# Optimization experiments

Hardware: AMD Instinct MI355X
Metric: run time of the kernel (lower is better)

The kernel has to match this reference:

```python
import jax, jax.numpy as jnp
from jax import lax
import numpy as np

EPS = 1e-06


def conv1x1(x, W, b):
    # x: [B,C,H,W], W: [O,C], b: [O]
    return jnp.einsum('bchw,oc->bohw', x, W) + b[None, :, None, None]


def conv3x3(x, W, b):
    # W: [O,I,3,3], 'SAME' padding
    y = lax.conv_general_dilated(x, W, (1, 1), 'SAME',
                                 dimension_numbers=('NCHW', 'OIHW', 'NCHW'))
    return y + b[None, :, None, None]


def setup_inputs() -> dict:
    key = jax.random.key(0)
    ks = jax.random.split(key, 13)
    B, C, H, W = 8, 64, 256, 256
    kc, vc = 64, 64
    s = 0.05
    return {
        'x':  jax.random.normal(ks[0], (B, C, H, W), jnp.float32),
        'Wq': jax.random.normal(ks[1], (kc, C), jnp.float32) * s,
        'bq': jax.random.normal(ks[2], (kc,), jnp.float32) * s,
        'Wk': jax.random.normal(ks[3], (kc, C), jnp.float32) * s,
        'bk': jax.random.normal(ks[4], (kc,), jnp.float32) * s,
        'Wv': jax.random.normal(ks[5], (vc, C), jnp.float32) * s,
        'bv': jax.random.normal(ks[6], (vc,), jnp.float32) * s,
        'Wr': jax.random.normal(ks[7], (C, vc), jnp.float32) * s,
        'br': jax.random.normal(ks[8], (C,), jnp.float32) * s,
        'W1': jax.random.normal(ks[9], (C, C, 3, 3), jnp.float32) * s,
        'b1': jax.random.normal(ks[10], (C,), jnp.float32) * s,
        'W2': jax.random.normal(ks[11], (C, C, 3, 3), jnp.float32) * s,
        'b2': jax.random.normal(ks[12], (C,), jnp.float32) * s,
    }


def reference(x, Wq, bq, Wk, bk, Wv, bv, Wr, br, W1, b1, W2, b2):
    B, C, H, W = x.shape
    N = H * W
    kc = Wq.shape[0]
    vc = Wv.shape[0]

    Q = conv1x1(x, Wq, bq).reshape(B, kc, N)
    K = conv1x1(x, Wk, bk).reshape(B, kc, N)
    V = conv1x1(x, Wv, bv).reshape(B, vc, N)

    # L2-normalize over the channel axis (dim=-2 in torch)
    Qn = Q / jnp.linalg.norm(Q, axis=1, keepdims=True)   # [B,kc,N]
    Kn = K / jnp.linalg.norm(K, axis=1, keepdims=True)   # [B,kc,N]
    Qt = jnp.transpose(Qn, (0, 2, 1))                     # [B,N,kc]

    # denominator: 1 / (N + Q . (sum_n K + eps))
    k_sum = Kn.sum(axis=-1) + EPS                         # [B,kc]
    denom = 1.0 / (N + jnp.einsum('bnc,bc->bn', Qt, k_sum))  # [B,N]

    value_sum = V.sum(axis=-1, keepdims=True)             # [B,vc,1]

    # linear-attention aggregation: KV^T then Q.(KV)
    agg_kv = jnp.einsum('bmn,bcn->bmc', Kn, V)            # [B,kc,vc]
    # the per-batch/per-head torch loop sums head slices of the full kc
    # contraction -> equivalent to a single einsum over kc
    agg_qkv = jnp.einsum('bmc,bnm->bcn', agg_kv, Qt)      # [B,vc,N]

    numerator = value_sum + agg_qkv                       # [B,vc,N]
    weight_value = (numerator * denom[:, None, :]).reshape(B, vc, H, W)

    attn = conv1x1(weight_value, Wr, br)                  # [B,C,H,W]
    out = conv3x3(conv3x3(attn, W1, b1), W2, b2) * x + x
    return out
```

## Files before the change

### kernel.cpp

```cpp
#include <hip/hip_runtime.h>

typedef __attribute__((ext_vector_type(8))) short short8;
typedef __attribute__((ext_vector_type(4))) float f32x4;
typedef __attribute__((ext_vector_type(4))) int i32x4;

#define NPIX 65536
#define KPITCH 264
#define RED_KSUM 0
#define RED_VSUM 512
#define RED_AGG 1024

__device__ __forceinline__ float b2f(unsigned short u) {
  union { unsigned int i; float f; } z; z.i = ((unsigned int)u) << 16; return z.f;
}
__device__ __forceinline__ unsigned short f2b(float f) {
  union { float f; unsigned int i; } z; z.f = f;
  unsigned int r = z.i + 0x7fffu + ((z.i >> 16) & 1u);
  return (unsigned short)(r >> 16);
}
__device__ __forceinline__ unsigned int packbf(float a, float b) {
  return (unsigned int)f2b(a) | ((unsigned int)f2b(b) << 16);
}
__device__ __forceinline__ int cvtpk(float a, float b) {
  int r;
  asm("v_cvt_pk_bf16_f32 %0, %1, %2" : "=v"(r) : "v"(a), "v"(b));
  return r;
}

__global__ __launch_bounds__(256) void prep_kernel(
    const float* __restrict__ W1, const float* __restrict__ W2,
    unsigned short* __restrict__ wA, float* __restrict__ red)
{
  const int i = blockIdx.x * 256 + threadIdx.x;
  if (i < 73728) {
    const float* W = (i < 36864) ? W1 : W2;
    const int e = (i < 36864) ? i : (i - 36864);
    const int j    = e & 7;
    const int lane = (e >> 3) & 63;
    const int mt   = (e >> 9) & 3;
    const int kb   = (e >> 11) & 1;
    const int tap  = e >> 12;
    const int o = mt * 16 + (lane & 15);
    const int c = kb * 32 + ((lane >> 4) << 3) + j;
    wA[i] = f2b(W[o * 576 + c * 9 + tap]);
  } else if (i < 73728 + 33792) {
    red[i - 73728] = 0.0f;
  }
}

#define PROJ(WM, BM)                                                           \
    {                                                                          \
      _Pragma("unroll")                                                        \
      for (int mt = 0; mt < 4; ++mt) {                                         \
        const f32x4 bb = *(const f32x4*)((BM) + mt * 16 + g * 4);              \
        _Pragma("unroll")                                                      \
        for (int nt = 0; nt < 4; ++nt) acc[mt][nt] = bb;                       \
      }                                                                        \
      _Pragma("unroll")                                                        \
      for (int kb = 0; kb < 2; ++kb) {                                         \
        short8 af[4];                                                          \
        _Pragma("unroll")                                                      \
        for (int mt = 0; mt < 4; ++mt) {                                       \
          const float* wp = (WM) + mt * 1024 + wrow + kb * 32;                 \
          const f32x4 w0 = *(const f32x4*)wp;                                  \
          const f32x4 w1 = *(const f32x4*)(wp + 4);                            \
          union { i32x4 i; short8 s; } uw;                                     \
          uw.i.x = cvtpk(w0.x, w0.y); uw.i.y = cvtpk(w0.z, w0.w);              \
          uw.i.z = cvtpk(w1.x, w1.y); uw.i.w = cvtpk(w1.z, w1.w);              \
          af[mt] = uw.s;                                                       \
        }                                                                      \
        _Pragma("unroll")                                                      \
        for (int mt = 0; mt < 4; ++mt)                                         \
          _Pragma("unroll")                                                    \
          for (int nt = 0; nt < 4; ++nt)                                       \
            acc[mt][nt] = __builtin_amdgcn_mfma_f32_16x16x32_bf16(             \
                af[mt], bf[nt][kb], acc[mt][nt], 0, 0, 0);                     \
      }                                                                        \
    }

__global__ __launch_bounds__(256, 2) void qkv_kernel(
    const float* __restrict__ x,
    const float* __restrict__ Wq, const float* __restrict__ bq,
    const float* __restrict__ Wk, const float* __restrict__ bk,
    const float* __restrict__ Wv, const float* __restrict__ bv,
    unsigned short* __restrict__ Qn, float* __restrict__ red)
{
  __shared__ __align__(16) unsigned short sh[2 * 64 * KPITCH];
  unsigned short* ks = sh;
  unsigned short* vs = sh + 64 * KPITCH;
  unsigned int* shu = (unsigned int*)sh;
  const int b = blockIdx.y;
  const int t = threadIdx.x;
  const int w = t >> 6;
  const int l = t & 63;
  const int g = l >> 4;
  const int l15 = l & 15;
  const int wrow = l15 * 64 + g * 8;
  const size_t xb = (size_t)b * 64 * NPIX;

  const f32x4 zero = {0.f, 0.f, 0.f, 0.f};
  f32x4 agg[4]  = {zero, zero, zero, zero};
  f32x4 kacc[4] = {zero, zero, zero, zero};
  f32x4 vacc[4] = {zero, zero, zero, zero};

  for (int it = 0; it < 4; ++it) {
    const int pxw = (blockIdx.x << 10) + (it << 8) + (w << 6);

    short8 bf[4][2];
#pragma unroll
    for (int nt = 0; nt < 4; ++nt) {
      const float* xp = x + xb + (size_t)(g * 8) * NPIX + pxw + nt * 16 + l15;
#pragma unroll
      for (int kb = 0; kb < 2; ++kb) {
        float f[8];
#pragma unroll
        for (int j = 0; j < 8; ++j)
          f[j] = xp[(size_t)(kb * 32 + j) * NPIX];
        union { i32x4 i; short8 s; } u;
        u.i.x = cvtpk(f[0], f[1]); u.i.y = cvtpk(f[2], f[3]);
        u.i.z = cvtpk(f[4], f[5]); u.i.w = cvtpk(f[6], f[7]);
        bf[nt][kb] = u.s;
      }
    }

    f32x4 acc[4][4];

    PROJ(Wq, bq);
    {
      float rq[4];
#pragma unroll
      for (int nt = 0; nt < 4; ++nt) {
        float ss = 0.f;
#pragma unroll
        for (int mt = 0; mt < 4; ++mt)
#pragma unroll
          for (int r = 0; r < 4; ++r)
            ss = fmaf(acc[mt][nt][r], acc[mt][nt][r], ss);
        ss += __shfl_xor(ss, 16);
        ss += __shfl_xor(ss, 32);
        rq[nt] = rsqrtf(ss);
      }
      unsigned int* sw = shu + w * 2304;
#pragma unroll
      for (int mt = 0; mt < 4; ++mt)
#pragma unroll
        for (int nt = 0; nt < 4; ++nt) {
          const int px = nt * 16 + l15;
          unsigned int* dst = sw + px * 36 + mt * 8 + g * 2;
          dst[0] = (unsigned)cvtpk(acc[mt][nt][0] * rq[nt], acc[mt][nt][1] * rq[nt]);
          dst[1] = (unsigned)cvtpk(acc[mt][nt][2] * rq[nt], acc[mt][nt][3] * rq[nt]);
        }
      const uint4* rr4 = (const uint4*)(shu + w * 2304);
#pragma unroll
      for (int k8 = 0; k8 < 8; ++k8) {
        const int p = (k8 << 3) + (l >> 3);
        const int ch8 = l & 7;
        *(uint4*)(Qn + ((size_t)b * NPIX + pxw + p) * 64 + ch8 * 8) =
            rr4[p * 9 + ch8];
      }
      __syncthreads();
    }

    PROJ(Wk, bk);
    {
      float rk[4];
#pragma unroll
      for (int nt = 0; nt < 4; ++nt) {
        float ss = 0.f;
#pragma unroll
        for (int mt = 0; mt < 4; ++mt)
#pragma unroll
          for (int r = 0; r < 4; ++r)
            ss = fmaf(acc[mt][nt][r], acc[mt][nt][r], ss);
        ss += __shfl_xor(ss, 16);
        ss += __shfl_xor(ss, 32);
        rk[nt] = rsqrtf(ss);
      }
#pragma unroll
      for (int mt = 0; mt < 4; ++mt)
#pragma unroll
        for (int nt = 0; nt < 4; ++nt)
#pragma unroll
          for (int r = 0; r < 4; ++r) {
            const float kn = acc[mt][nt][r] * rk[nt];
            kacc[mt][r] += kn;
            ks[(mt * 16 + g * 4 + r) * KPITCH + (w << 6) + nt * 16 + l15] =
                (unsigned short)cvtpk(kn, 0.f);
          }
    }

    PROJ(Wv, bv);
    {
#pragma unroll
      for (int mt = 0; mt < 4; ++mt)
#pragma unroll
        for (int nt = 0; nt < 4; ++nt)
#pragma unroll
          for (int r = 0; r < 4; ++r) {
            const float vv = acc[mt][nt][r];
            vacc[mt][r] += vv;
            vs[(mt * 16 + g * 4 + r) * KPITCH + (w << 6) + nt * 16 + l15] =
                (unsigned short)cvtpk(vv, 0.f);
          }
    }
    __syncthreads();

#pragma unroll
    for (int s = 0; s < 8; ++s) {
      const short8 ak =
          *(const short8*)(ks + (w * 16 + l15) * KPITCH + s * 32 + g * 8);
#pragma unroll
      for (int nt = 0; nt < 4; ++nt) {
        const short8 bv8 =
            *(const short8*)(vs + (nt * 16 + l15) * KPITCH + s * 32 + g * 8);
        agg[nt] = __builtin_amdgcn_mfma_f32_16x16x32_bf16(ak, bv8, agg[nt], 0, 0, 0);
      }
    }
    __syncthreads();
  }

#pragma unroll
  for (int mt = 0; mt < 4; ++mt)
#pragma unroll
    for (int r = 0; r < 4; ++r) {
      float kv = kacc[mt][r], vv = vacc[mt][r];
#pragma unroll
      for (int d = 1; d < 16; d <<= 1) {
        kv += __shfl_xor(kv, d);
        vv += __shfl_xor(vv, d);
      }
      if (l15 == 0) {
        atomicAdd(red + RED_KSUM + b * 64 + mt * 16 + g * 4 + r, kv);
        atomicAdd(red + RED_VSUM + b * 64 + mt * 16 + g * 4 + r, vv);
      }
    }
  float* ab = red + RED_AGG + b * 4096;
#pragma unroll
  for (int nt = 0; nt < 4; ++nt)
#pragma unroll
    for (int r = 0; r < 4; ++r)
      atomicAdd(ab + (w * 16 + g * 4 + r) * 64 + nt * 16 + l15, agg[nt][r]);
}

__global__ __launch_bounds__(256) void prep2_kernel(
    const float* __restrict__ Wr, const float* __restrict__ red,
    unsigned short* __restrict__ Cb, float* __restrict__ u,
    float* __restrict__ ks2)
{
  const int b = blockIdx.y;
  const int t = threadIdx.x;
  const int o = t & 63;
  const int kq = t >> 6;
  const float* wr = Wr + o * 64;
  const float* agg = red + RED_AGG + b * 4096;
#pragma unroll
  for (int i = 0; i < 4; ++i) {
    const int k = blockIdx.x * 16 + kq * 4 + i;
    const float* ar = agg + k * 64;
    float s = 0.f;
#pragma unroll
    for (int v = 0; v < 64; ++v) s = fmaf(wr[v], ar[v], s);
    const int mt = o >> 4, kb = k >> 5;
    const int lane = (o & 15) | (((k >> 3) & 3) << 4);
    const int j = k & 7;
    const unsigned short c1 = f2b(s);
    const float r1 = s - b2f(c1);
    Cb[b * 4096 + ((kb * 4 + mt) * 64 + lane) * 8 + j] = c1;
    Cb[32768 + b * 4096 + ((kb * 4 + mt) * 64 + lane) * 8 + j] = f2b(r1);
  }
  if (blockIdx.x == 0 && t < 64) {
    const float* vsr = red + RED_VSUM + b * 64;
    float s = 0.f;
#pragma unroll
    for (int v = 0; v < 64; ++v) s = fmaf(Wr[t * 64 + v], vsr[v], s);
    u[b * 64 + t] = s;
    ks2[b * 64 + t] = red[RED_KSUM + b * 64 + t] + 1e-6f;
  }
}

__global__ __launch_bounds__(256, 2) void attn_kernel(
    const unsigned short* __restrict__ Qn,
    const unsigned short* __restrict__ Cb,
    const float* __restrict__ u,
    const float* __restrict__ ks2,
    const float* __restrict__ br,
    unsigned short* __restrict__ attn)
{
  __shared__ __align__(16) unsigned short att[256 * 72];
  const int b = blockIdx.y;
  const int t = threadIdx.x;
  const int w = t >> 6, l = t & 63, g = l >> 4, l15 = l & 15;

  short8 af[2][2][4];
#pragma unroll
  for (int lvl = 0; lvl < 2; ++lvl)
#pragma unroll
    for (int kb = 0; kb < 2; ++kb)
#pragma unroll
      for (int mt = 0; mt < 4; ++mt)
        af[lvl][kb][mt] = *(const short8*)(
            Cb + lvl * 32768 + b * 4096 + ((kb * 4 + mt) * 64 + l) * 8);
  f32x4 uu[4], brf[4];
#pragma unroll
  for (int mt = 0; mt < 4; ++mt) {
    uu[mt]  = *(const f32x4*)(u + b * 64 + mt * 16 + g * 4);
    brf[mt] = *(const f32x4*)(br + mt * 16 + g * 4);
  }
  float ksl[16];
#pragma unroll
  for (int kb = 0; kb < 2; ++kb)
#pragma unroll
    for (int j = 0; j < 8; ++j)
      ksl[kb * 8 + j] = ks2[b * 64 + kb * 32 + g * 8 + j];

  for (int it = 0; it < 4; ++it) {
    const int pxw = (blockIdx.x << 10) + (it << 8) + (w << 6);
    short8 qf[4][2];
    float denom[4];
#pragma unroll
    for (int nt = 0; nt < 4; ++nt) {
      const unsigned short* qp =
          Qn + ((size_t)b * NPIX + pxw + nt * 16 + l15) * 64 + g * 8;
      qf[nt][0] = *(const short8*)qp;
      qf[nt][1] = *(const short8*)(qp + 32);
      float ss = 0.f;
#pragma unroll
      for (int kb = 0; kb < 2; ++kb)
#pragma unroll
        for (int j = 0; j < 8; ++j)
          ss = fmaf(b2f((unsigned short)qf[nt][kb][j]), ksl[kb * 8 + j], ss);
      ss += __shfl_xor(ss, 16);
      ss += __shfl_xor(ss, 32);
      denom[nt] = 1.0f / (65536.0f + ss);
    }
    f32x4 acc[4][4];
#pragma unroll
    for (int mt = 0; mt < 4; ++mt)
#pragma unroll
      for (int nt = 0; nt < 4; ++nt) acc[mt][nt] = uu[mt];
#pragma unroll
    for (int kb = 0; kb < 2; ++kb)
#pragma unroll
      for (int mt = 0; mt < 4; ++mt)
#pragma unroll
        for (int nt = 0; nt < 4; ++nt) {
          acc[mt][nt] = __builtin_amdgcn_mfma_f32_16x16x32_bf16(
              af[0][kb][mt], qf[nt][kb], acc[mt][nt], 0, 0, 0);
          acc[mt][nt] = __builtin_amdgcn_mfma_f32_16x16x32_bf16(
              af[1][kb][mt], qf[nt][kb], acc[mt][nt], 0, 0, 0);
        }
    unsigned int* sw = (unsigned int*)att + w * 2304;
#pragma unroll
    for (int mt = 0; mt < 4; ++mt)
#pragma unroll
      for (int nt = 0; nt < 4; ++nt) {
        const int px = nt * 16 + l15;
        unsigned int* dst = sw + px * 36 + mt * 8 + g * 2;
        dst[0] = (unsigned)cvtpk(fmaf(acc[mt][nt][0], denom[nt], brf[mt][0]),
                                 fmaf(acc[mt][nt][1], denom[nt], brf[mt][1]));
        dst[1] = (unsigned)cvtpk(fmaf(acc[mt][nt][2], denom[nt], brf[mt][2]),
                                 fmaf(acc[mt][nt][3], denom[nt], brf[mt][3]));
      }
    const uint4* rr4 = (const uint4*)att + w * 576;
#pragma unroll
    for (int k8 = 0; k8 < 8; ++k8) {
      const int p = (k8 << 3) + (l >> 3);
      const int ch8 = l & 7;
      *(uint4*)(attn + ((size_t)b * NPIX + pxw + p) * 64 + ch8 * 8) =
          rr4[p * 9 + ch8];
    }
  }
}

template <int EPI>
__global__ __launch_bounds__(256, 3) void conv3_kernel(
    const unsigned short* __restrict__ in,
    const unsigned short* __restrict__ wA,
    const float* __restrict__ bias,
    const float* __restrict__ xin,
    unsigned short* __restrict__ outh,
    float* __restrict__ outf)
{
  __shared__ __align__(16) unsigned short tile[10 * 34 * 72];
  const int bz = blockIdx.z;
  const int ty0 = blockIdx.y << 3;
  const int tx0 = blockIdx.x << 5;
  const int tid = threadIdx.x;
  const size_t nb = (size_t)bz * NPIX;

  for (int s = tid; s < 2720; s += 256) {
    const int g = s & 7;
    const int pix = s >> 3;
    const int xx = pix % 34;
    const int row = pix / 34;
    const int gx = tx0 + xx - 1;
    const int gy = ty0 + row - 1;
    uint4 v = {0u, 0u, 0u, 0u};
    if ((unsigned)gx < 256u && (unsigned)gy < 256u)
      v = *(const uint4*)(in + ((nb + (gy << 8) + gx) << 6) + (g << 3));
    *(uint4*)(tile + pix * 72 + (g << 3)) = v;
  }
  __syncthreads();

  const int w = tid >> 6, lane = tid & 63, q = lane >> 4, l = lane & 15;
  f32x4 acc[4][4];
  {
#pragma unroll
    for (int mt = 0; mt < 4; ++mt) {
      const f32x4 bb = *(const f32x4*)(bias + mt * 16 + q * 4);
#pragma unroll
      for (int nt = 0; nt < 4; ++nt) acc[mt][nt] = bb;
    }
  }
  const short8* tp = (const short8*)tile;
  for (int tap = 0; tap < 9; ++tap) {
    const int dy = tap / 3, dx = tap - dy * 3;
#pragma unroll
    for (int kb = 0; kb < 2; ++kb) {
      const unsigned short* wp = wA + (tap * 2 + kb) * 2048 + lane * 8;
      short8 af[4];
#pragma unroll
      for (int mt = 0; mt < 4; ++mt) af[mt] = *(const short8*)(wp + mt * 512);
      short8 bf[4];
#pragma unroll
      for (int nt = 0; nt < 4; ++nt) {
        const int yl = (w << 1) + (nt >> 1) + dy;
        const int xl = ((nt & 1) << 4) + l + dx;
        bf[nt] = tp[(yl * 34 + xl) * 9 + (kb << 2) + q];
      }
#pragma unroll
      for (int mt = 0; mt < 4; ++mt)
#pragma unroll
        for (int nt = 0; nt < 4; ++nt)
          acc[mt][nt] = __builtin_amdgcn_mfma_f32_16x16x32_bf16(
              af[mt], bf[nt], acc[mt][nt], 0, 0, 0);
    }
  }

  if (EPI == 0) {
    __syncthreads();
    unsigned int* wreg = (unsigned int*)tile + w * 2304;
#pragma unroll
    for (int mt = 0; mt < 4; ++mt)
#pragma unroll
      for (int nt = 0; nt < 4; ++nt) {
        const int p = ((nt >> 1) << 5) + ((nt & 1) << 4) + l;
        unsigned int* dst = wreg + p * 36 + (mt << 3) + (q << 1);
        dst[0] = packbf(acc[mt][nt][0], acc[mt][nt][1]);
        dst[1] = packbf(acc[mt][nt][2], acc[mt][nt][3]);
      }
    __syncthreads();
    const uint4* rreg = (const uint4*)tile + w * 576;
#pragma unroll
    for (int k = 0; k < 8; ++k) {
      const int p = (k << 3) + (lane >> 3);
      const int ch = lane & 7;
      const int gx = tx0 + (p & 31);
      const int gy = ty0 + (w << 1) + (p >> 5);
      *(uint4*)(outh + ((nb + (gy << 8) + gx) << 6) + (ch << 3)) =
          rreg[p * 9 + ch];
    }
  } else {
#pragma unroll
    for (int mt = 0; mt < 4; ++mt)
#pragma unroll
      for (int nt = 0; nt < 4; ++nt) {
        const int gx = tx0 + ((nt & 1) << 4) + l;
        const int gy = ty0 + (w << 1) + (nt >> 1);
#pragma unroll
        for (int r = 0; r < 4; ++r) {
          const int o = (mt << 4) + (q << 2) + r;
          const size_t idx = (((size_t)bz * 64 + o) << 16) + (gy << 8) + gx;
          const float xo = xin[idx];
          outf[idx] = fmaf(acc[mt][nt][r], xo, xo);
        }
      }
  }
}

extern "C" void kernel_launch(void* const* d_in, const int* in_sizes, int n_in,
                              void* d_out, int out_size, void* d_ws, size_t ws_size,
                              hipStream_t stream) {
  (void)in_sizes; (void)n_in; (void)out_size; (void)ws_size;
  const float* x  = (const float*)d_in[0];
  const float* Wq = (const float*)d_in[1];
  const float* bq = (const float*)d_in[2];
  const float* Wk = (const float*)d_in[3];
  const float* bk = (const float*)d_in[4];
  const float* Wv = (const float*)d_in[5];
  const float* bv = (const float*)d_in[6];
  const float* Wr = (const float*)d_in[7];
  const float* br = (const float*)d_in[8];
  const float* W1 = (const float*)d_in[9];
  const float* b1 = (const float*)d_in[10];
  const float* W2 = (const float*)d_in[11];
  const float* b2 = (const float*)d_in[12];

  unsigned short* wA1 = (unsigned short*)d_ws;
  unsigned short* wA2 = wA1 + 36864;
  float* red = (float*)((char*)d_ws + 147456);
  unsigned short* bufA = (unsigned short*)((char*)d_ws + 294912);
  unsigned short* Cb = (unsigned short*)((char*)d_ws + 294912);
  float* u_  = (float*)((char*)d_ws + 294912 + 131072);
  float* ks2 = (float*)((char*)d_ws + 294912 + 133120);
  unsigned short* bufB = (unsigned short*)d_out;
  unsigned short* bufQ = (unsigned short*)((char*)d_out + 67108864);

  prep_kernel<<<420, 256, 0, stream>>>(W1, W2, wA1, red);
  qkv_kernel<<<dim3(64, 8), 256, 0, stream>>>(x, Wq, bq, Wk, bk, Wv, bv, bufQ, red);
  prep2_kernel<<<dim3(4, 8), 256, 0, stream>>>(Wr, red, Cb, u_, ks2);
  attn_kernel<<<dim3(64, 8), 256, 0, stream>>>(bufQ, Cb, u_, ks2, br, bufB);
  conv3_kernel<0><<<dim3(8, 32, 8), 256, 0, stream>>>(
      bufB, wA1, b1, nullptr, bufA, nullptr);
  conv3_kernel<1><<<dim3(8, 32, 8), 256, 0, stream>>>(
      bufA, wA2, b2, x, nullptr, (float*)d_out);
}
```

Before: 599.1 us.

## Eliminate V projection by aggregating x-weighted K norms and folding Wv in prep2

The qkv kernel no longer computes the V projection or stores normalized K and V in shared memory. Instead it accumulates M = sum over pixels of (x scaled by 1/||K||) times x^T, plus per-channel sums, and prep2 reconstructs agg_kv, k_sum and value_sum algebraically through Wk, Wv, bk and bv. This removes a projection's worth of MFMA work and a large shared-memory staging buffer, which lets occupancy rise to 3 blocks per CU. In exchange it re-reads x from global memory, changes the bf16 rounding points, and makes prep2 a serial 8-block matrix chain.

```diff
diff --git a/kernel.cpp b/kernel.cpp
--- a/kernel.cpp
+++ b/kernel.cpp
@@ -5,10 +5,10 @@
 typedef __attribute__((ext_vector_type(4))) int i32x4;
 
 #define NPIX 65536
-#define KPITCH 264
-#define RED_KSUM 0
-#define RED_VSUM 512
+#define RED_M1 0
+#define RED_MX 512
 #define RED_AGG 1024
+#define RED_S1 33792
 
 __device__ __forceinline__ float b2f(unsigned short u) {
   union { unsigned int i; float f; } z; z.i = ((unsigned int)u) << 16; return z.f;
@@ -43,7 +43,7 @@
     const int o = mt * 16 + (lane & 15);
     const int c = kb * 32 + ((lane >> 4) << 3) + j;
     wA[i] = f2b(W[o * 576 + c * 9 + tap]);
-  } else if (i < 73728 + 33792) {
+  } else if (i < 73728 + 33800) {
     red[i - 73728] = 0.0f;
   }
 }
@@ -78,33 +78,27 @@
       }                                                                        \
     }
 
-__global__ __launch_bounds__(256, 2) void qkv_kernel(
+__global__ __launch_bounds__(256, 3) void qkv_kernel(
     const float* __restrict__ x,
     const float* __restrict__ Wq, const float* __restrict__ bq,
     const float* __restrict__ Wk, const float* __restrict__ bk,
-    const float* __restrict__ Wv, const float* __restrict__ bv,
     unsigned short* __restrict__ Qn, float* __restrict__ red)
 {
-  __shared__ __align__(16) unsigned short sh[2 * 64 * KPITCH];
-  unsigned short* ks = sh;
-  unsigned short* vs = sh + 64 * KPITCH;
-  unsigned int* shu = (unsigned int*)sh;
+  __shared__ __align__(16) unsigned short qsc[4 * 2304];
+  __shared__ __align__(16) float dkbuf[256];
   const int b = blockIdx.y;
   const int t = threadIdx.x;
-  const int w = t >> 6;
-  const int l = t & 63;
-  const int g = l >> 4;
-  const int l15 = l & 15;
+  const int w = t >> 6, l = t & 63, g = l >> 4, l15 = l & 15;
   const int wrow = l15 * 64 + g * 8;
   const size_t xb = (size_t)b * 64 * NPIX;
 
   const f32x4 zero = {0.f, 0.f, 0.f, 0.f};
-  f32x4 agg[4]  = {zero, zero, zero, zero};
-  f32x4 kacc[4] = {zero, zero, zero, zero};
-  f32x4 vacc[4] = {zero, zero, zero, zero};
+  f32x4 Mw[4] = {zero, zero, zero, zero};
+  float m1p = 0.f, mxp = 0.f, s1p = 0.f;
 
   for (int it = 0; it < 4; ++it) {
-    const int pxw = (blockIdx.x << 10) + (it << 8) + (w << 6);
+    const int pxblk = (blockIdx.x << 10) + (it << 8);
+    const int pxw = pxblk + (w << 6);
 
     short8 bf[4][2];
 #pragma unroll
@@ -140,25 +134,29 @@
         ss += __shfl_xor(ss, 32);
         rq[nt] = rsqrtf(ss);
       }
-      unsigned int* sw = shu + w * 2304;
-#pragma unroll
-      for (int mt = 0; mt < 4; ++mt)
-#pragma unroll
-        for (int nt = 0; nt < 4; ++nt) {
-          const int px = nt * 16 + l15;
-          unsigned int* dst = sw + px * 36 + mt * 8 + g * 2;
-          dst[0] = (unsigned)cvtpk(acc[mt][nt][0] * rq[nt], acc[mt][nt][1] * rq[nt]);
-          dst[1] = (unsigned)cvtpk(acc[mt][nt][2] * rq[nt], acc[mt][nt][3] * rq[nt]);
+      unsigned int* sw = (unsigned int*)qsc + w * 1152;
+#pragma unroll
+      for (int h = 0; h < 2; ++h) {
+#pragma unroll
+        for (int mt = 0; mt < 4; ++mt)
+#pragma unroll
+          for (int n2 = 0; n2 < 2; ++n2) {
+            const int nt = h * 2 + n2;
+            unsigned int* dst = sw + (n2 * 16 + l15) * 36 + mt * 8 + g * 2;
+            dst[0] = (unsigned)cvtpk(acc[mt][nt][0] * rq[nt],
+                                     acc[mt][nt][1] * rq[nt]);
+            dst[1] = (unsigned)cvtpk(acc[mt][nt][2] * rq[nt],
+                                     acc[mt][nt][3] * rq[nt]);
+          }
+        const uint4* rr4 = (const uint4*)qsc + w * 288;
+#pragma unroll
+        for (int k4 = 0; k4 < 4; ++k4) {
+          const int p = (k4 << 3) + (l >> 3);
+          const int ch8 = l & 7;
+          *(uint4*)(Qn + ((size_t)b * NPIX + pxw + h * 32 + p) * 64 + ch8 * 8) =
+              rr4[p * 9 + ch8];
         }
-      const uint4* rr4 = (const uint4*)(shu + w * 2304);
-#pragma unroll
-      for (int k8 = 0; k8 < 8; ++k8) {
-        const int p = (k8 << 3) + (l >> 3);
-        const int ch8 = l & 7;
-        *(uint4*)(Qn + ((size_t)b * NPIX + pxw + p) * 64 + ch8 * 8) =
-            rr4[p * 9 + ch8];
-      }
-      __syncthreads();
+      }
     }
 
     PROJ(Wk, bk);
@@ -176,105 +174,135 @@
         ss += __shfl_xor(ss, 32);
         rk[nt] = rsqrtf(ss);
       }
-#pragma unroll
-      for (int mt = 0; mt < 4; ++mt)
+      s1p += rk[0] + rk[1] + rk[2] + rk[3];
+      if (l < 16) {
 #pragma unroll
         for (int nt = 0; nt < 4; ++nt)
-#pragma unroll
-          for (int r = 0; r < 4; ++r) {
-            const float kn = acc[mt][nt][r] * rk[nt];
-            kacc[mt][r] += kn;
-            ks[(mt * 16 + g * 4 + r) * KPITCH + (w << 6) + nt * 16 + l15] =
-                (unsigned short)cvtpk(kn, 0.f);
-          }
-    }
-
-    PROJ(Wv, bv);
-    {
-#pragma unroll
-      for (int mt = 0; mt < 4; ++mt)
-#pragma unroll
-        for (int nt = 0; nt < 4; ++nt)
-#pragma unroll
-          for (int r = 0; r < 4; ++r) {
-            const float vv = acc[mt][nt][r];
-            vacc[mt][r] += vv;
-            vs[(mt * 16 + g * 4 + r) * KPITCH + (w << 6) + nt * 16 + l15] =
-                (unsigned short)cvtpk(vv, 0.f);
-          }
+          dkbuf[(w << 6) + nt * 16 + l15] = rk[nt];
+      }
     }
     __syncthreads();
 
 #pragma unroll
     for (int s = 0; s < 8; ++s) {
-      const short8 ak =
-          *(const short8*)(ks + (w * 16 + l15) * KPITCH + s * 32 + g * 8);
-#pragma unroll
-      for (int nt = 0; nt < 4; ++nt) {
-        const short8 bv8 =
-            *(const short8*)(vs + (nt * 16 + l15) * KPITCH + s * 32 + g * 8);
-        agg[nt] = __builtin_amdgcn_mfma_f32_16x16x32_bf16(ak, bv8, agg[nt], 0, 0, 0);
+      const int pk = pxblk + s * 32 + g * 8;
+      const float* xa = x + xb + (size_t)(w * 16 + l15) * NPIX + pk;
+      const f32x4 a0 = *(const f32x4*)xa;
+      const f32x4 a1 = *(const f32x4*)(xa + 4);
+      const f32x4 d0 = *(const f32x4*)(dkbuf + s * 32 + g * 8);
+      const f32x4 d1 = *(const f32x4*)(dkbuf + s * 32 + g * 8 + 4);
+      const float p0 = a0.x * d0.x, p1 = a0.y * d0.y;
+      const float p2 = a0.z * d0.z, p3 = a0.w * d0.w;
+      const float p4 = a1.x * d1.x, p5 = a1.y * d1.y;
+      const float p6 = a1.z * d1.z, p7 = a1.w * d1.w;
+      m1p += p0 + p1 + p2 + p3 + p4 + p5 + p6 + p7;
+      mxp += a0.x + a0.y + a0.z + a0.w + a1.x + a1.y + a1.z + a1.w;
+      union { i32x4 i; short8 s8; } ua;
+      ua.i.x = cvtpk(p0, p1); ua.i.y = cvtpk(p2, p3);
+      ua.i.z = cvtpk(p4, p5); ua.i.w = cvtpk(p6, p7);
+#pragma unroll
+      for (int nt = 0; nt < 4; ++nt) {
+        const float* xbp = x + xb + (size_t)(nt * 16 + l15) * NPIX + pk;
+        const f32x4 b0 = *(const f32x4*)xbp;
+        const f32x4 b1 = *(const f32x4*)(xbp + 4);
+        union { i32x4 i; short8 s8; } ub;
+        ub.i.x = cvtpk(b0.x, b0.y); ub.i.y = cvtpk(b0.z, b0.w);
+        ub.i.z = cvtpk(b1.x, b1.y); ub.i.w = cvtpk(b1.z, b1.w);
+        Mw[nt] = __builtin_amdgcn_mfma_f32_16x16x32_bf16(
+            ua.s8, ub.s8, Mw[nt], 0, 0, 0);
       }
     }
     __syncthreads();
   }
 
-#pragma unroll
-  for (int mt = 0; mt < 4; ++mt)
-#pragma unroll
-    for (int r = 0; r < 4; ++r) {
-      float kv = kacc[mt][r], vv = vacc[mt][r];
-#pragma unroll
-      for (int d = 1; d < 16; d <<= 1) {
-        kv += __shfl_xor(kv, d);
-        vv += __shfl_xor(vv, d);
-      }
-      if (l15 == 0) {
-        atomicAdd(red + RED_KSUM + b * 64 + mt * 16 + g * 4 + r, kv);
-        atomicAdd(red + RED_VSUM + b * 64 + mt * 16 + g * 4 + r, vv);
-      }
-    }
-  float* ab = red + RED_AGG + b * 4096;
+  m1p += __shfl_xor(m1p, 16); m1p += __shfl_xor(m1p, 32);
+  mxp += __shfl_xor(mxp, 16); mxp += __shfl_xor(mxp, 32);
+  if (l < 16) {
+    atomicAdd(red + RED_M1 + b * 64 + w * 16 + l15, m1p);
+    atomicAdd(red + RED_MX + b * 64 + w * 16 + l15, mxp);
+  }
+  s1p += __shfl_xor(s1p, 1); s1p += __shfl_xor(s1p, 2);
+  s1p += __shfl_xor(s1p, 4); s1p += __shfl_xor(s1p, 8);
+  if (l == 0) atomicAdd(red + RED_S1 + b, s1p);
+  float* Mb = red + RED_AGG + b * 4096;
 #pragma unroll
   for (int nt = 0; nt < 4; ++nt)
 #pragma unroll
     for (int r = 0; r < 4; ++r)
-      atomicAdd(ab + (w * 16 + g * 4 + r) * 64 + nt * 16 + l15, agg[nt][r]);
+      atomicAdd(Mb + (w * 16 + g * 4 + r) * 64 + nt * 16 + l15, Mw[nt][r]);
 }
 
 __global__ __launch_bounds__(256) void prep2_kernel(
+    const float* __restrict__ Wk, const float* __restrict__ bk,
+    const float* __restrict__ Wv, const float* __restrict__ bv,
     const float* __restrict__ Wr, const float* __restrict__ red,
     unsigned short* __restrict__ Cb, float* __restrict__ u,
     float* __restrict__ ks2)
 {
-  const int b = blockIdx.y;
+  __shared__ float T[4096];
+  __shared__ float P2[4096];
+  __shared__ float sm[320];
+  const int b = blockIdx.x;
   const int t = threadIdx.x;
-  const int o = t & 63;
-  const int kq = t >> 6;
-  const float* wr = Wr + o * 64;
-  const float* agg = red + RED_AGG + b * 4096;
-#pragma unroll
-  for (int i = 0; i < 4; ++i) {
-    const int k = blockIdx.x * 16 + kq * 4 + i;
-    const float* ar = agg + k * 64;
-    float s = 0.f;
-#pragma unroll
-    for (int v = 0; v < 64; ++v) s = fmaf(wr[v], ar[v], s);
-    const int mt = o >> 4, kb = k >> 5;
-    const int lane = (o & 15) | (((k >> 3) & 3) << 4);
-    const int j = k & 7;
-    const unsigned short c1 = f2b(s);
-    const float r1 = s - b2f(c1);
-    Cb[b * 4096 + ((kb * 4 + mt) * 64 + lane) * 8 + j] = c1;
-    Cb[32768 + b * 4096 + ((kb * 4 + mt) * 64 + lane) * 8 + j] = f2b(r1);
-  }
-  if (blockIdx.x == 0 && t < 64) {
-    const float* vsr = red + RED_VSUM + b * 64;
-    float s = 0.f;
-#pragma unroll
-    for (int v = 0; v < 64; ++v) s = fmaf(Wr[t * 64 + v], vsr[v], s);
-    u[b * 64 + t] = s;
-    ks2[b * 64 + t] = red[RED_KSUM + b * 64 + t] + 1e-6f;
+  const float* M  = red + RED_AGG + b * 4096;
+  const float* m1 = red + RED_M1 + b * 64;
+  const float* mx = red + RED_MX + b * 64;
+  const float s1 = red[RED_S1 + b];
+  if (t < 64) {
+    float a = 0.f, c = 0.f, d = 0.f;
+    for (int v = 0; v < 64; ++v) {
+      a = fmaf(Wk[t * 64 + v], m1[v], a);
+      c = fmaf(Wv[t * 64 + v], m1[v], c);
+      d = fmaf(Wv[t * 64 + v], mx[v], d);
+    }
+    sm[t] = a;
+    sm[64 + t] = c;
+    sm[128 + t] = d;
+  }
+  __syncthreads();
+  {
+    const int o = t & 63, n0 = (t >> 6) * 16;
+    for (int n = n0; n < n0 + 16; ++n) {
+      float s = 0.f;
+      for (int v = 0; v < 64; ++v) s = fmaf(Wv[o * 64 + v], M[v * 64 + n], s);
+      T[o * 64 + n] = s;
+    }
+  }
+  __syncthreads();
+  {
+    const int o = t & 63, n0 = (t >> 6) * 16;
+    for (int n = n0; n < n0 + 16; ++n) {
+      float s = 0.f;
+      for (int v = 0; v < 64; ++v) s = fmaf(Wr[o * 64 + v], T[v * 64 + n], s);
+      P2[o * 64 + n] = s;
+    }
+  }
+  if (t < 64) {
+    float t3 = 0.f, uu = 0.f, e2 = 0.f;
+    for (int v = 0; v < 64; ++v) {
+      t3 = fmaf(Wr[t * 64 + v], bv[v], t3);
+      uu = fmaf(Wr[t * 64 + v], sm[128 + v], uu);
+      e2 = fmaf(Wr[t * 64 + v], sm[64 + v], e2);
+    }
+    u[b * 64 + t] = uu + 65536.0f * t3;
+    ks2[b * 64 + t] = sm[t] + s1 * bk[t] + 1e-6f;
+    sm[192 + t] = t3;
+    sm[256 + t] = e2 + s1 * t3;
+  }
+  __syncthreads();
+  {
+    const int o = t & 63, k0 = (t >> 6) * 16;
+    for (int k = k0; k < k0 + 16; ++k) {
+      float s = fmaf(sm[192 + o], sm[k], sm[256 + o] * bk[k]);
+      for (int v = 0; v < 64; ++v) s = fmaf(P2[o * 64 + v], Wk[k * 64 + v], s);
+      const int mt = o >> 4, kb = k >> 5;
+      const int lane = (o & 15) | (((k >> 3) & 3) << 4);
+      const int j = k & 7;
+      const unsigned short c1 = f2b(s);
+      const float r1 = s - b2f(c1);
+      Cb[b * 4096 + ((kb * 4 + mt) * 64 + lane) * 8 + j] = c1;
+      Cb[32768 + b * 4096 + ((kb * 4 + mt) * 64 + lane) * 8 + j] = f2b(r1);
+    }
   }
 }
 
@@ -506,9 +534,9 @@
   unsigned short* bufB = (unsigned short*)d_out;
   unsigned short* bufQ = (unsigned short*)((char*)d_out + 67108864);
 
-  prep_kernel<<<420, 256, 0, stream>>>(W1, W2, wA1, red);
-  qkv_kernel<<<dim3(64, 8), 256, 0, stream>>>(x, Wq, bq, Wk, bk, Wv, bv, bufQ, red);
-  prep2_kernel<<<dim3(4, 8), 256, 0, stream>>>(Wr, red, Cb, u_, ks2);
+  prep_kernel<<<421, 256, 0, stream>>>(W1, W2, wA1, red);
+  qkv_kernel<<<dim3(64, 8), 256, 0, stream>>>(x, Wq, bq, Wk, bk, bufQ, red);
+  prep2_kernel<<<8, 256, 0, stream>>>(Wk, bk, Wv, bv, Wr, red, Cb, u_, ks2);
   attn_kernel<<<dim3(64, 8), 256, 0, stream>>>(bufQ, Cb, u_, ks2, br, bufB);
   conv3_kernel<0><<<dim3(8, 32, 8), 256, 0, stream>>>(
       bufB, wA1, b1, nullptr, bufA, nullptr);
```

Measured after the change: 720.0 us. +20.2%, slower.

## Halve per-wave pixel tile in QKV kernel and prefetch next x tile

Applied to the files above, without the earlier changes.

The QKV projection kernel now handles 32 pixels per wave per round instead of 64 and launches twice as many blocks. Launch bounds are raised to 4 blocks per SM, and shared memory shrinks accordingly. The x tile for the next round is loaded right after the K/V shared-memory sync, so global loads overlap the KV aggregation MFMAs. The aim is more occupancy and more latency hiding on the memory-bound x read. In exchange each block repeats its weight conversions more often, and the reduction atomics double.

```diff
diff --git a/kernel.cpp b/kernel.cpp
--- a/kernel.cpp
+++ b/kernel.cpp
@@ -5,7 +5,7 @@
 typedef __attribute__((ext_vector_type(4))) int i32x4;
 
 #define NPIX 65536
-#define KPITCH 264
+#define KP 136
 #define RED_KSUM 0
 #define RED_VSUM 512
 #define RED_AGG 1024
@@ -48,13 +48,31 @@
   }
 }
 
-#define PROJ(WM, BM)                                                           \
+#define LOADBF(PX)                                                             \
+    {                                                                          \
+      _Pragma("unroll")                                                        \
+      for (int nt = 0; nt < 2; ++nt) {                                         \
+        const float* xp = x + xb + (size_t)(g * 8) * NPIX + (PX) + nt * 16 + l15; \
+        _Pragma("unroll")                                                      \
+        for (int kb = 0; kb < 2; ++kb) {                                       \
+          float f[8];                                                          \
+          _Pragma("unroll")                                                    \
+          for (int j = 0; j < 8; ++j)                                          \
+            f[j] = xp[(size_t)(kb * 32 + j) * NPIX];                           \
+          union { i32x4 i; short8 s; } u2;                                     \
+          u2.i.x = cvtpk(f[0], f[1]); u2.i.y = cvtpk(f[2], f[3]);              \
+          u2.i.z = cvtpk(f[4], f[5]); u2.i.w = cvtpk(f[6], f[7]);              \
+          bf[nt][kb] = u2.s;                                                   \
+        }                                                                      \
+      }                                                                        \
+    }
+
+#define PROJ2(WM, BM)                                                          \
     {                                                                          \
       _Pragma("unroll")                                                        \
       for (int mt = 0; mt < 4; ++mt) {                                         \
         const f32x4 bb = *(const f32x4*)((BM) + mt * 16 + g * 4);              \
-        _Pragma("unroll")                                                      \
-        for (int nt = 0; nt < 4; ++nt) acc[mt][nt] = bb;                       \
+        acc[mt][0] = bb; acc[mt][1] = bb;                                      \
       }                                                                        \
       _Pragma("unroll")                                                        \
       for (int kb = 0; kb < 2; ++kb) {                                         \
@@ -72,29 +90,25 @@
         _Pragma("unroll")                                                      \
         for (int mt = 0; mt < 4; ++mt)                                         \
           _Pragma("unroll")                                                    \
-          for (int nt = 0; nt < 4; ++nt)                                       \
+          for (int nt = 0; nt < 2; ++nt)                                       \
             acc[mt][nt] = __builtin_amdgcn_mfma_f32_16x16x32_bf16(             \
                 af[mt], bf[nt][kb], acc[mt][nt], 0, 0, 0);                     \
       }                                                                        \
     }
 
-__global__ __launch_bounds__(256, 2) void qkv_kernel(
+__global__ __launch_bounds__(256, 4) void qkv_kernel(
     const float* __restrict__ x,
     const float* __restrict__ Wq, const float* __restrict__ bq,
     const float* __restrict__ Wk, const float* __restrict__ bk,
     const float* __restrict__ Wv, const float* __restrict__ bv,
     unsigned short* __restrict__ Qn, float* __restrict__ red)
 {
-  __shared__ __align__(16) unsigned short sh[2 * 64 * KPITCH];
+  __shared__ __align__(16) unsigned short sh[2 * 64 * KP];
   unsigned short* ks = sh;
-  unsigned short* vs = sh + 64 * KPITCH;
-  unsigned int* shu = (unsigned int*)sh;
+  unsigned short* vs = sh + 64 * KP;
   const int b = blockIdx.y;
   const int t = threadIdx.x;
-  const int w = t >> 6;
-  const int l = t & 63;
-  const int g = l >> 4;
-  const int l15 = l & 15;
+  const int w = t >> 6, l = t & 63, g = l >> 4, l15 = l & 15;
   const int wrow = l15 * 64 + g * 8;
   const size_t xb = (size_t)b * 64 * NPIX;
 
@@ -103,33 +117,20 @@
   f32x4 kacc[4] = {zero, zero, zero, zero};
   f32x4 vacc[4] = {zero, zero, zero, zero};
 
-  for (int it = 0; it < 4; ++it) {
-    const int pxw = (blockIdx.x << 10) + (it << 8) + (w << 6);
-
-    short8 bf[4][2];
-#pragma unroll
-    for (int nt = 0; nt < 4; ++nt) {
-      const float* xp = x + xb + (size_t)(g * 8) * NPIX + pxw + nt * 16 + l15;
-#pragma unroll
-      for (int kb = 0; kb < 2; ++kb) {
-        float f[8];
-#pragma unroll
-        for (int j = 0; j < 8; ++j)
-          f[j] = xp[(size_t)(kb * 32 + j) * NPIX];
-        union { i32x4 i; short8 s; } u;
-        u.i.x = cvtpk(f[0], f[1]); u.i.y = cvtpk(f[2], f[3]);
-        u.i.z = cvtpk(f[4], f[5]); u.i.w = cvtpk(f[6], f[7]);
-        bf[nt][kb] = u.s;
-      }
-    }
-
-    f32x4 acc[4][4];
-
-    PROJ(Wq, bq);
+  short8 bf[2][2];
+  LOADBF((blockIdx.x << 9) + (w << 5));
+
+  for (int rd = 0; rd < 4; ++rd) {
+    const int pxblk = (blockIdx.x << 9) + (rd << 7);
+    const int pxw = pxblk + (w << 5);
+
+    f32x4 acc[4][2];
+
+    PROJ2(Wq, bq);
     {
-      float rq[4];
-#pragma unroll
-      for (int nt = 0; nt < 4; ++nt) {
+      float rq[2];
+#pragma unroll
+      for (int nt = 0; nt < 2; ++nt) {
         float ss = 0.f;
 #pragma unroll
         for (int mt = 0; mt < 4; ++mt)
@@ -140,32 +141,33 @@
         ss += __shfl_xor(ss, 32);
         rq[nt] = rsqrtf(ss);
       }
-      unsigned int* sw = shu + w * 2304;
+      unsigned int* sw = (unsigned int*)sh + w * 1152;
 #pragma unroll
       for (int mt = 0; mt < 4; ++mt)
 #pragma unroll
-        for (int nt = 0; nt < 4; ++nt) {
-          const int px = nt * 16 + l15;
-          unsigned int* dst = sw + px * 36 + mt * 8 + g * 2;
-          dst[0] = (unsigned)cvtpk(acc[mt][nt][0] * rq[nt], acc[mt][nt][1] * rq[nt]);
-          dst[1] = (unsigned)cvtpk(acc[mt][nt][2] * rq[nt], acc[mt][nt][3] * rq[nt]);
+        for (int nt = 0; nt < 2; ++nt) {
+          unsigned int* dst = sw + (nt * 16 + l15) * 36 + mt * 8 + g * 2;
+          dst[0] = (unsigned)cvtpk(acc[mt][nt][0] * rq[nt],
+                                   acc[mt][nt][1] * rq[nt]);
+          dst[1] = (unsigned)cvtpk(acc[mt][nt][2] * rq[nt],
+                                   acc[mt][nt][3] * rq[nt]);
         }
-      const uint4* rr4 = (const uint4*)(shu + w * 2304);
-#pragma unroll
-      for (int k8 = 0; k8 < 8; ++k8) {
-        const int p = (k8 << 3) + (l >> 3);
+      const uint4* rr4 = (const uint4*)sh + w * 288;
+#pragma unroll
+      for (int k4 = 0; k4 < 4; ++k4) {
+        const int p = (k4 << 3) + (l >> 3);
         const int ch8 = l & 7;
         *(uint4*)(Qn + ((size_t)b * NPIX + pxw + p) * 64 + ch8 * 8) =
             rr4[p * 9 + ch8];
       }
-      __syncthreads();
-    }
-
-    PROJ(Wk, bk);
+    }
+    __syncthreads();
+
+    PROJ2(Wk, bk);
     {
-      float rk[4];
-#pragma unroll
-      for (int nt = 0; nt < 4; ++nt) {
+      float rk[2];
+#pragma unroll
+      for (int nt = 0; nt < 2; ++nt) {
         float ss = 0.f;
 #pragma unroll
         for (int mt = 0; mt < 4; ++mt)
@@ -179,41 +181,44 @@
 #pragma unroll
       for (int mt = 0; mt < 4; ++mt)
 #pragma unroll
-        for (int nt = 0; nt < 4; ++nt)
+        for (int nt = 0; nt < 2; ++nt)
 #pragma unroll
           for (int r = 0; r < 4; ++r) {
             const float kn = acc[mt][nt][r] * rk[nt];
             kacc[mt][r] += kn;
-            ks[(mt * 16 + g * 4 + r) * KPITCH + (w << 6) + nt * 16 + l15] =
+            ks[(mt * 16 + g * 4 + r) * KP + (w << 5) + nt * 16 + l15] =
                 (unsigned short)cvtpk(kn, 0.f);
           }
     }
 
-    PROJ(Wv, bv);
+    PROJ2(Wv, bv);
     {
 #pragma unroll
       for (int mt = 0; mt < 4; ++mt)
 #pragma unroll
-        for (int nt = 0; nt < 4; ++nt)
+        for (int nt = 0; nt < 2; ++nt)
 #pragma unroll
           for (int r = 0; r < 4; ++r) {
             const float vv = acc[mt][nt][r];
             vacc[mt][r] += vv;
-            vs[(mt * 16 + g * 4 + r) * KPITCH + (w << 6) + nt * 16 + l15] =
+            vs[(mt * 16 + g * 4 + r) * KP + (w << 5) + nt * 16 + l15] =
                 (unsigned short)cvtpk(vv, 0.f);
           }
     }
     __syncthreads();
 
-#pragma unroll
-    for (int s = 0; s < 8; ++s) {
+    if (rd < 3) LOADBF(pxblk + 128 + (w << 5));
+
+#pragma unroll
+    for (int s = 0; s < 4; ++s) {
       const short8 ak =
-          *(const short8*)(ks + (w * 16 + l15) * KPITCH + s * 32 + g * 8);
-#pragma unroll
-      for (int nt = 0; nt < 4; ++nt) {
+          *(const short8*)(ks + (w * 16 + l15) * KP + s * 32 + g * 8);
+#pragma unroll
+      for (int nt2 = 0; nt2 < 4; ++nt2) {
         const short8 bv8 =
-            *(const short8*)(vs + (nt * 16 + l15) * KPITCH + s * 32 + g * 8);
-        agg[nt] = __builtin_amdgcn_mfma_f32_16x16x32_bf16(ak, bv8, agg[nt], 0, 0, 0);
+            *(const short8*)(vs + (nt2 * 16 + l15) * KP + s * 32 + g * 8);
+        agg[nt2] = __builtin_amdgcn_mfma_f32_16x16x32_bf16(
+            ak, bv8, agg[nt2], 0, 0, 0);
       }
     }
     __syncthreads();
@@ -507,7 +512,7 @@
   unsigned short* bufQ = (unsigned short*)((char*)d_out + 67108864);
 
   prep_kernel<<<420, 256, 0, stream>>>(W1, W2, wA1, red);
-  qkv_kernel<<<dim3(64, 8), 256, 0, stream>>>(x, Wq, bq, Wk, bk, Wv, bv, bufQ, red);
+  qkv_kernel<<<dim3(128, 8), 256, 0, stream>>>(x, Wq, bq, Wk, bk, Wv, bv, bufQ, red);
   prep2_kernel<<<dim3(4, 8), 256, 0, stream>>>(Wr, red, Cb, u_, ks2);
   attn_kernel<<<dim3(64, 8), 256, 0, stream>>>(bufQ, Cb, u_, ks2, br, bufB);
   conv3_kernel<0><<<dim3(8, 32, 8), 256, 0, stream>>>(
```

Result: slower. 749.0 us (+25.0%).
